# Kernel tuning notes

Measured on AMD Instinct MI355X. Metric: run time of the kernel, lower is better.

Reference implementation:

```python
import jax, jax.numpy as jnp
import numpy as np

B, N, F, OUT = 32768, 512, 8, 32


def setup_inputs() -> dict:
    key = jax.random.key(0)
    ks = jax.random.split(key, 9)
    ego_summary = jax.random.normal(ks[0], (B, F), dtype=jnp.float32)
    neighbors = jax.random.normal(ks[1], (B, N, F), dtype=jnp.float32)
    mask = jax.random.randint(ks[2], (B, N), 0, 2).astype(bool)
    s_ego = 1.0 / np.sqrt(F)
    s_attn = 1.0 / np.sqrt(2 * F)
    W_ego = jax.random.uniform(ks[3], (F, F), minval=-s_ego, maxval=s_ego)
    b_ego = jax.random.uniform(ks[4], (F,), minval=-s_ego, maxval=s_ego)
    w_attn = jax.random.uniform(ks[5], (2 * F,), minval=-s_attn, maxval=s_attn)
    b_attn = jax.random.uniform(ks[6], (1,), minval=-s_attn, maxval=s_attn)
    W_out = jax.random.uniform(ks[7], (F, OUT), minval=-s_ego, maxval=s_ego)
    b_out = jax.random.uniform(ks[8], (OUT,), minval=-s_ego, maxval=s_ego)
    return {"ego_summary": ego_summary, "neighbors": neighbors, "mask": mask,
            "W_ego": W_ego, "b_ego": b_ego, "w_attn": w_attn, "b_attn": b_attn,
            "W_out": W_out, "b_out": b_out}


def reference(ego_summary, neighbors, mask, W_ego, b_ego, w_attn, b_attn, W_out, b_out):
    f = W_ego.shape[0]
    # ego projection: [B, F]
    ego_p = ego_summary @ W_ego + b_ego
    # attn Linear(2F, 1) on concat([ego_exp, neighbors]) == split weight, no concat
    wa_e, wa_n = w_attn[:f], w_attn[f:]
    scores = (ego_p @ wa_e)[:, None] + neighbors @ wa_n + b_attn[0]  # [B, N]
    NEG = jnp.float32(-1e9)
    scores = jnp.where(mask, scores, NEG)
    all_masked = ~jnp.any(mask, axis=-1, keepdims=True)  # [B, 1]
    scores = jnp.where(all_masked, jnp.float32(0.0), scores)
    weights = jax.nn.softmax(scores, axis=-1) * mask.astype(scores.dtype)  # [B, N]
    agg = jnp.einsum('bn,bnf->bf', weights, neighbors)  # [B, F]
    return agg @ W_out + b_out  # [B, OUT]
```

## Files before the change

kernel.cpp:

```cpp
#include <hip/hip_runtime.h>
#include <stdint.h>

__global__ __launch_bounds__(256) void gat_kernel(
    const float* __restrict__ ego,
    const float* __restrict__ neigh,
    const int*   __restrict__ mask,
    const float* __restrict__ W_ego,
    const float* __restrict__ b_ego,
    const float* __restrict__ w_attn,
    const float* __restrict__ b_attn,
    const float* __restrict__ W_out,
    const float* __restrict__ b_out,
    float* __restrict__ out,
    int B)
{
    const int lane = threadIdx.x & 63;
    const int row  = (blockIdx.x << 2) + (threadIdx.x >> 6);
    if (row >= B) return;

    float e = b_attn[0];
    #pragma unroll
    for (int fp = 0; fp < 8; ++fp) {
        float ep = b_ego[fp];
        #pragma unroll
        for (int f = 0; f < 8; ++f)
            ep = fmaf(ego[row * 8 + f], W_ego[f * 8 + fp], ep);
        e = fmaf(ep, w_attn[fp], e);
    }

    float wn[8];
    #pragma unroll
    for (int f = 0; f < 8; ++f) wn[f] = w_attn[8 + f];

    const float4* __restrict__ nrow = (const float4*)(neigh + (size_t)row * (512 * 8));
    const int*    __restrict__ mrow = mask + (size_t)row * 512;

    float x[8][8];
    float s[8];
    bool  valid[8];
    #pragma unroll
    for (int j = 0; j < 8; ++j) {
        const int n = (j << 6) + lane;
        const float4 a = nrow[2 * n];
        const float4 b = nrow[2 * n + 1];
        x[j][0] = a.x; x[j][1] = a.y; x[j][2] = a.z; x[j][3] = a.w;
        x[j][4] = b.x; x[j][5] = b.y; x[j][6] = b.z; x[j][7] = b.w;
        valid[j] = (mrow[n] != 0);
        float d = e;
        #pragma unroll
        for (int f = 0; f < 8; ++f) d = fmaf(x[j][f], wn[f], d);
        s[j] = valid[j] ? d : -1.0e9f;
    }

    float m = s[0];
    #pragma unroll
    for (int j = 1; j < 8; ++j) m = fmaxf(m, s[j]);
    #pragma unroll
    for (int off = 32; off > 0; off >>= 1) m = fmaxf(m, __shfl_xor(m, off));

    float Z = 0.0f;
    float agg[8] = {0.f, 0.f, 0.f, 0.f, 0.f, 0.f, 0.f, 0.f};
    #pragma unroll
    for (int j = 0; j < 8; ++j) {
        const float w = valid[j] ? __expf(s[j] - m) : 0.0f;
        Z += w;
        #pragma unroll
        for (int f = 0; f < 8; ++f) agg[f] = fmaf(w, x[j][f], agg[f]);
    }
    #pragma unroll
    for (int off = 32; off > 0; off >>= 1) {
        Z += __shfl_xor(Z, off);
        #pragma unroll
        for (int f = 0; f < 8; ++f) agg[f] += __shfl_xor(agg[f], off);
    }

    const float inv = (Z > 0.0f) ? (1.0f / Z) : 0.0f;

    if (lane < 32) {
        float o = b_out[lane];
        #pragma unroll
        for (int f = 0; f < 8; ++f)
            o = fmaf(agg[f] * inv, W_out[f * 32 + lane], o);
        out[(size_t)row * 32 + lane] = o;
    }
}

extern "C" void kernel_launch(void* const* d_in, const int* in_sizes, int n_in,
                              void* d_out, int out_size, void* d_ws, size_t ws_size,
                              hipStream_t stream) {
    const float* ego    = (const float*)d_in[0];
    const float* neigh  = (const float*)d_in[1];
    const int*   mask   = (const int*)d_in[2];
    const float* W_ego  = (const float*)d_in[3];
    const float* b_ego  = (const float*)d_in[4];
    const float* w_attn = (const float*)d_in[5];
    const float* b_attn = (const float*)d_in[6];
    const float* W_out  = (const float*)d_in[7];
    const float* b_out  = (const float*)d_in[8];
    float* out = (float*)d_out;

    const int B = in_sizes[0] / 8;
    const int grid = (B + 3) / 4;

    gat_kernel<<<grid, 256, 0, stream>>>(ego, neigh, mask, W_ego, b_ego,
                                         w_attn, b_attn, W_out, b_out, out, B);
}
```

Measured before the change: 720.3 us.

## Use online softmax with double-buffered neighbor loads to cut register pressure

Replaces the two-pass softmax, which held all 64 neighbor values per lane in registers, with a per-lane online softmax that rescales running max, sum and aggregate. Neighbor and mask loads are software-pipelined two tiles ahead, and launch bounds now request 6 waves-per-EU-level occupancy. The aim is fewer registers and more waves in flight to hide memory latency on this bandwidth-bound kernel. In exchange it adds extra exp calls per element and a more expensive cross-lane merge with rescaling.

```diff
diff --git a/kernel.cpp b/kernel.cpp
--- a/kernel.cpp
+++ b/kernel.cpp
@@ -1,7 +1,7 @@
 #include <hip/hip_runtime.h>
 #include <stdint.h>
 
-__global__ __launch_bounds__(256) void gat_kernel(
+__global__ __launch_bounds__(256, 6) void gat_kernel(
     const float* __restrict__ ego,
     const float* __restrict__ neigh,
     const int*   __restrict__ mask,
@@ -35,43 +35,57 @@
     const float4* __restrict__ nrow = (const float4*)(neigh + (size_t)row * (512 * 8));
     const int*    __restrict__ mrow = mask + (size_t)row * 512;
 
-    float x[8][8];
-    float s[8];
-    bool  valid[8];
+    float m = -1.0e9f;
+    float Z = 0.0f;
+    float agg[8] = {0.f, 0.f, 0.f, 0.f, 0.f, 0.f, 0.f, 0.f};
+
+    float4 a0 = nrow[2 * lane];
+    float4 b0 = nrow[2 * lane + 1];
+    int    v0 = mrow[lane];
+    float4 a1 = nrow[2 * (64 + lane)];
+    float4 b1 = nrow[2 * (64 + lane) + 1];
+    int    v1 = mrow[64 + lane];
+
     #pragma unroll
     for (int j = 0; j < 8; ++j) {
-        const int n = (j << 6) + lane;
-        const float4 a = nrow[2 * n];
-        const float4 b = nrow[2 * n + 1];
-        x[j][0] = a.x; x[j][1] = a.y; x[j][2] = a.z; x[j][3] = a.w;
-        x[j][4] = b.x; x[j][5] = b.y; x[j][6] = b.z; x[j][7] = b.w;
-        valid[j] = (mrow[n] != 0);
+        const float4 a = a0; const float4 b = b0; const int vv = v0;
+        a0 = a1; b0 = b1; v0 = v1;
+        if (j < 6) {
+            const int n = ((j + 2) << 6) + lane;
+            a1 = nrow[2 * n];
+            b1 = nrow[2 * n + 1];
+            v1 = mrow[n];
+        }
+
+        const float xf[8] = {a.x, a.y, a.z, a.w, b.x, b.y, b.z, b.w};
         float d = e;
         #pragma unroll
-        for (int f = 0; f < 8; ++f) d = fmaf(x[j][f], wn[f], d);
-        s[j] = valid[j] ? d : -1.0e9f;
+        for (int f = 0; f < 8; ++f) d = fmaf(xf[f], wn[f], d);
+        const float s = vv ? d : -1.0e9f;
+
+        const float mn = fmaxf(m, s);
+        const float c  = __expf(m - mn);
+        const float w  = vv ? __expf(s - mn) : 0.0f;
+        Z = fmaf(Z, c, w);
+        #pragma unroll
+        for (int f = 0; f < 8; ++f) agg[f] = fmaf(agg[f], c, w * xf[f]);
+        m = mn;
     }
 
-    float m = s[0];
-    #pragma unroll
-    for (int j = 1; j < 8; ++j) m = fmaxf(m, s[j]);
-    #pragma unroll
-    for (int off = 32; off > 0; off >>= 1) m = fmaxf(m, __shfl_xor(m, off));
-
-    float Z = 0.0f;
-    float agg[8] = {0.f, 0.f, 0.f, 0.f, 0.f, 0.f, 0.f, 0.f};
-    #pragma unroll
-    for (int j = 0; j < 8; ++j) {
-        const float w = valid[j] ? __expf(s[j] - m) : 0.0f;
-        Z += w;
-        #pragma unroll
-        for (int f = 0; f < 8; ++f) agg[f] = fmaf(w, x[j][f], agg[f]);
-    }
     #pragma unroll
     for (int off = 32; off > 0; off >>= 1) {
-        Z += __shfl_xor(Z, off);
+        const float m2 = __shfl_xor(m, off);
+        const float Z2 = __shfl_xor(Z, off);
+        float ag2[8];
         #pragma unroll
-        for (int f = 0; f < 8; ++f) agg[f] += __shfl_xor(agg[f], off);
+        for (int f = 0; f < 8; ++f) ag2[f] = __shfl_xor(agg[f], off);
+        const float mn = fmaxf(m, m2);
+        const float c1 = __expf(m - mn);
+        const float c2 = __expf(m2 - mn);
+        Z = Z * c1 + Z2 * c2;
+        #pragma unroll
+        for (int f = 0; f < 8; ++f) agg[f] = agg[f] * c1 + ag2[f] * c2;
+        m = mn;
     }
 
     const float inv = (Z > 0.0f) ? (1.0f / Z) : 0.0f;
```

New measurement: 718.5 us. About the same (-0.2%).
